# Optimization experiments

Measured on AMD Instinct MI355X. Metric: run time of the kernel, lower is better.

## Reference

```python
import jax, jax.numpy as jnp
import numpy as np

B, S, D_IN, D_OUT, N, R = 8, 4096, 1280, 1280, 4, 16


def setup_inputs() -> dict:
    key = jax.random.key(0)
    ks = jax.random.split(key, 7)
    x = jax.random.normal(ks[0], (B, S, D_IN), dtype=jnp.float32)
    W = jax.random.normal(ks[1], (D_OUT, D_IN), dtype=jnp.float32) * 0.02
    bias = jax.random.normal(ks[2], (D_OUT,), dtype=jnp.float32) * 0.02
    A = jax.random.normal(ks[3], (N, R, D_IN), dtype=jnp.float32) * 0.02
    Bw = jax.random.normal(ks[4], (N, D_OUT, R), dtype=jnp.float32) * 0.02
    scalings = jax.random.uniform(ks[5], (N,), dtype=jnp.float32)
    masks = jax.random.uniform(ks[6], (N, S), dtype=jnp.float32)
    # normalize masks to sum ~1 per position, per docstring
    masks = masks / jnp.sum(masks, axis=0, keepdims=True)
    return {"x": x, "W": W, "bias": bias, "A": A, "Bw": Bw,
            "scalings": scalings, "masks": masks}


def reference(x, W, bias, A, Bw, scalings, masks):
    # base linear: y = x @ W^T + b
    base = jnp.einsum('bsd,od->bso', x, W) + bias
    # batched LoRA branches: h = x @ A_i^T  (b,s,n,r)
    h = jnp.einsum('bsd,nrd->bsnr', x, A)
    # lora_out_i = h @ B_i^T  (b,s,n,o)
    lora = jnp.einsum('bsnr,nor->bsno', h, Bw)
    # weighted sum over subjects: scaling_i * mask_i(pos)
    lora_sum = jnp.einsum('bsno,n,ns->bso', lora, scalings, masks)
    return base + lora_sum
```

## Files before the change

kernel.cpp:

```cpp
#include <hip/hip_runtime.h>
#include <hip/hip_bf16.h>
#include <stdint.h>

#define S_LEN   4096
#define DIN     1280
#define DOUT    1280
#define N_LORA  4
#define R_LORA  16
#define M_TOT   32768
#define KC      (DIN + N_LORA*R_LORA)
#define NR      64

typedef __attribute__((ext_vector_type(4))) float floatx4;
typedef __attribute__((ext_vector_type(8))) short shortx8;

typedef union { uint4 u; shortx8 s; } punx8;

static __device__ __forceinline__ unsigned short bf16_rne(float f) {
    union { float f; unsigned u; } v; v.f = f;
    unsigned u = v.u;
    u += 0x7fffu + ((u >> 16) & 1u);
    return (unsigned short)(u >> 16);
}

static __device__ __forceinline__ void async16(const unsigned short* g, unsigned short* l) {
    __builtin_amdgcn_global_load_lds(
        (const __attribute__((address_space(1))) unsigned int*)g,
        (__attribute__((address_space(3))) unsigned int*)l, 16, 0, 0);
}

static __device__ __forceinline__ uint4 cvt8(const float* src) {
    const float4* p = (const float4*)src;
    float4 a = p[0], b = p[1];
    uint4 o;
    o.x = (unsigned)bf16_rne(a.x) | ((unsigned)bf16_rne(a.y) << 16);
    o.y = (unsigned)bf16_rne(a.z) | ((unsigned)bf16_rne(a.w) << 16);
    o.z = (unsigned)bf16_rne(b.x) | ((unsigned)bf16_rne(b.y) << 16);
    o.w = (unsigned)bf16_rne(b.z) | ((unsigned)bf16_rne(b.w) << 16);
    return o;
}

#define VMCNT(n) asm volatile("s_waitcnt vmcnt(" #n ")" ::: "memory")
#define LGKM0    do { asm volatile("s_waitcnt lgkmcnt(0)" ::: "memory"); \
                      __builtin_amdgcn_sched_barrier(0); } while (0)
static __device__ __forceinline__ void barx() {
    asm volatile("" ::: "memory");
    __builtin_amdgcn_s_barrier();
    asm volatile("" ::: "memory");
}

__global__ __launch_bounds__(256) void k_build_wcat(const float* __restrict__ W,
                                                    const float* __restrict__ Bw,
                                                    unsigned short* __restrict__ Wcat) {
    int i = blockIdx.x * 256 + threadIdx.x;
    int e = i * 8;
    int o = e / KC;
    int c = e - o * KC;
    const float* src;
    if (c < DIN) {
        src = W + o * DIN + c;
    } else {
        int j = c - DIN;
        int n = j >> 4, r = j & 15;
        src = Bw + (n * DOUT + o) * R_LORA + r;
    }
    *(uint4*)(Wcat + o * KC + c) = cvt8(src);
}

__global__ __launch_bounds__(256) void k_convert_abp(const float* __restrict__ A,
                                                     unsigned short* __restrict__ Abp) {
    int step = blockIdx.x;
    int t = threadIdx.x;
    int ct = t >> 6, lane = t & 63;
    int mi = lane & 15, kq = lane >> 4;
    const float* src = A + (ct * 16 + mi) * DIN + step * 32 + kq * 8;
    *(uint4*)(Abp + ((size_t)(step * 4 + ct) * 64 + lane) * 8) = cvt8(src);
}

__global__ __launch_bounds__(1024) void k_lora_g(const float* __restrict__ x,
                                                 const unsigned short* __restrict__ Abp,
                                                 const float* __restrict__ scalings,
                                                 const float* __restrict__ masks,
                                                 unsigned short* __restrict__ g,
                                                 unsigned short* __restrict__ xb) {
    __shared__ float hs[4][64][64];
    int tid = threadIdx.x;
    int wave = tid >> 6, lane = tid & 63;
    int kg = wave >> 2, wv = wave & 3;
    int mi = lane & 15, kq = lane >> 4;
    int m0 = blockIdx.x * 64;

    const float* xrow = x + (size_t)(m0 + wv * 16 + mi) * DIN;
    unsigned short* xbrow = xb + (size_t)(m0 + wv * 16 + mi) * DIN;

    floatx4 acc[4] = {};
    for (int s = 0; s < 10; ++s) {
        int step = kg * 10 + s;
        int k = step * 32 + kq * 8;
        punx8 xp; xp.u = cvt8(xrow + k);
        *(uint4*)(xbrow + k) = xp.u;
        shortx8 xf = xp.s;
#pragma unroll
        for (int ct = 0; ct < 4; ++ct) {
            shortx8 bfr = *(const shortx8*)(Abp + ((size_t)(step * 4 + ct) * 64 + lane) * 8);
            acc[ct] = __builtin_amdgcn_mfma_f32_16x16x32_bf16(xf, bfr, acc[ct], 0, 0, 0);
        }
    }
#pragma unroll
    for (int ct = 0; ct < 4; ++ct)
#pragma unroll
        for (int reg = 0; reg < 4; ++reg)
            hs[kg][wv * 16 + kq * 4 + reg][ct * 16 + mi] = acc[ct][reg];
    __syncthreads();

    int r = tid >> 4;
    int c0 = (tid & 15) * 4;
    float4 s0 = *(const float4*)&hs[0][r][c0];
    float4 s1 = *(const float4*)&hs[1][r][c0];
    float4 s2 = *(const float4*)&hs[2][r][c0];
    float4 s3 = *(const float4*)&hs[3][r][c0];
    int n = c0 >> 4;
    int m = m0 + r;
    float wgt = scalings[n] * masks[n * S_LEN + (m & (S_LEN - 1))];
    float v0 = (s0.x + s1.x + s2.x + s3.x) * wgt;
    float v1 = (s0.y + s1.y + s2.y + s3.y) * wgt;
    float v2 = (s0.z + s1.z + s2.z + s3.z) * wgt;
    float v3 = (s0.w + s1.w + s2.w + s3.w) * wgt;
    uint2 packed;
    packed.x = (unsigned)bf16_rne(v0) | ((unsigned)bf16_rne(v1) << 16);
    packed.y = (unsigned)bf16_rne(v2) | ((unsigned)bf16_rne(v3) << 16);
    *(uint2*)(g + (size_t)m * NR + c0) = packed;
}

__global__ __launch_bounds__(512, 2) void k_main_gemm(const unsigned short* __restrict__ xb,
                                                      const unsigned short* __restrict__ g,
                                                      const unsigned short* __restrict__ Wcat,
                                                      const float* __restrict__ bias,
                                                      float* __restrict__ out) {
    __shared__ alignas(16) unsigned short As[2][256 * 64];
    __shared__ alignas(16) unsigned short Bs[2][256 * 64];

    const int tid = threadIdx.x;
    const int wave = tid >> 6, lane = tid & 63;
    const int wm = wave >> 2, wn = wave & 3;
    const int mi = lane & 15, kq = lane >> 4;

    int bx = blockIdx.x;
    int xcd = bx & 7, slot = bx >> 3;
    int srb = slot / 5;
    const int m0 = (xcd * 16 + srb) * 256;
    const int n0 = (slot - srb * 5) * 256;

    const int tr = tid >> 3;
    const int ts = (tid & 7) ^ (tr & 7);

    const unsigned short* pA = xb   + (size_t)(m0 + tr) * DIN + ts * 8;
    const unsigned short* pG = g    + (size_t)(m0 + tr) * NR  + ts * 8;
    const unsigned short* pB = Wcat + (size_t)(n0 + tr) * KC  + ts * 8;

    const int swz  = mi & 7;
    const int loK0 = mi * 128 + (((0) + kq) ^ swz) * 16;
    const int loK1 = mi * 128 + (((4) + kq) ^ swz) * 16;
    const int rbA  = (wm * 128) * 128;
    const int rbB  = (wn * 64) * 128;

    floatx4 acc[8][4] = {};
    shortx8 aR[2][8];
    shortx8 b[2][4];

    auto stA = [&](int t, int h) {
        unsigned short* d = &As[t & 1][(h * 128) * 64 + tid * 8];
        if (t < 20) {
            const unsigned short* s = pA + (size_t)(h * 128) * DIN + t * 64;
            async16(s, d);
            async16(s + (size_t)64 * DIN, d + 64 * 64);
        } else {
            const unsigned short* s = pG + (size_t)(h * 128) * NR;
            async16(s, d);
            async16(s + (size_t)64 * NR, d + 64 * 64);
        }
    };
    auto stB = [&](int t, int h) {
        const unsigned short* s = pB + (size_t)(h * 128) * KC + t * 64;
        unsigned short* d = &Bs[t & 1][(h * 128) * 64 + tid * 8];
        async16(s, d);
        async16(s + (size_t)64 * KC, d + 64 * 64);
    };

#define READ_A(bufb, mh)  _Pragma("unroll") \
    for (int fm = 0; fm < 4; ++fm) { \
        const char* p = (const char*)As[bufb] + rbA + ((mh) * 64 + fm * 16) * 128; \
        aR[(mh)][fm * 2 + 0] = *(const shortx8*)(p + loK0); \
        aR[(mh)][fm * 2 + 1] = *(const shortx8*)(p + loK1); \
    }
#define READ_B(bufb, nh)  _Pragma("unroll") \
    for (int fn = 0; fn < 2; ++fn) { \
        const char* p = (const char*)Bs[bufb] + rbB + ((nh) * 32 + fn * 16) * 128; \
        b[nh][fn * 2 + 0] = *(const shortx8*)(p + loK0); \
        b[nh][fn * 2 + 1] = *(const shortx8*)(p + loK1); \
    }
#define MFMA16(mh, nh)  do { __builtin_amdgcn_s_setprio(1); \
    _Pragma("unroll") \
    for (int fm = 0; fm < 4; ++fm) \
        _Pragma("unroll") \
        for (int fn = 0; fn < 2; ++fn) { \
            acc[(mh)*4+fm][(nh)*2+fn] = __builtin_amdgcn_mfma_f32_16x16x32_bf16( \
                aR[(mh)][fm*2+0], b[nh][fn*2+0], acc[(mh)*4+fm][(nh)*2+fn], 0, 0, 0); \
            acc[(mh)*4+fm][(nh)*2+fn] = __builtin_amdgcn_mfma_f32_16x16x32_bf16( \
                aR[(mh)][fm*2+1], b[nh][fn*2+1], acc[(mh)*4+fm][(nh)*2+fn], 0, 0, 0); \
        } \
    __builtin_amdgcn_s_setprio(0); } while (0)

    stA(0, 0); stA(0, 1); stB(0, 0); stB(0, 1);
    stB(1, 0); stB(1, 1); stA(1, 0);
    VMCNT(6);
    barx();
    READ_A(0, 0); READ_B(0, 0);

    for (int it = 0; it < 10; ++it) {
        const int T1 = 2 * it + 1, N0 = 2 * it + 2, N1 = 2 * it + 3;
        const bool lastI = (it == 9);

        barx();
        stA(T1, 1);
        LGKM0;
        READ_B(0, 1);
        MFMA16(0, 0);
        barx();
        LGKM0;
        READ_A(0, 1);
        MFMA16(0, 1);
        barx();
        stB(N0, 0);
        LGKM0;
        MFMA16(1, 0);
        VMCNT(2);
        barx();
        stB(N0, 1); stA(N0, 0);
        LGKM0;
        READ_A(1, 0); READ_B(1, 0);
        MFMA16(1, 1);
        barx();
        stA(N0, 1);
        LGKM0;
        READ_B(1, 1);
        MFMA16(0, 0);
        barx();
        LGKM0;
        READ_A(1, 1);
        MFMA16(0, 1);
        barx();
        if (!lastI) stB(N1, 0);
        LGKM0;
        MFMA16(1, 0);
        if (lastI) { VMCNT(0); } else { VMCNT(2); }
        barx();
        if (!lastI) { stB(N1, 1); stA(N1, 0); }
        LGKM0;
        READ_A(0, 0); READ_B(0, 0);
        MFMA16(1, 1);
    }

    LGKM0;
    READ_B(0, 1);
    MFMA16(0, 0);
    LGKM0;
    READ_A(0, 1);
    MFMA16(0, 1);
    LGKM0;
    MFMA16(1, 0);
    MFMA16(1, 1);

    float bv[4];
#pragma unroll
    for (int nf = 0; nf < 4; ++nf)
        bv[nf] = bias[n0 + wn * 64 + (nf >> 1) * 32 + (nf & 1) * 16 + mi];
#pragma unroll
    for (int mf = 0; mf < 8; ++mf) {
        const int row = m0 + wm * 128 + (mf >> 2) * 64 + (mf & 3) * 16 + kq * 4;
#pragma unroll
        for (int nf = 0; nf < 4; ++nf) {
            const int col = n0 + wn * 64 + (nf >> 1) * 32 + (nf & 1) * 16 + mi;
            float* op = out + (size_t)row * DOUT + col;
#pragma unroll
            for (int reg = 0; reg < 4; ++reg)
                op[(size_t)reg * DOUT] = acc[mf][nf][reg] + bv[nf];
        }
    }
#undef READ_A
#undef READ_B
#undef MFMA16
}

extern "C" void kernel_launch(void* const* d_in, const int* in_sizes, int n_in,
                              void* d_out, int out_size, void* d_ws, size_t ws_size,
                              hipStream_t stream) {
    const float* x     = (const float*)d_in[0];
    const float* W     = (const float*)d_in[1];
    const float* bias  = (const float*)d_in[2];
    const float* A     = (const float*)d_in[3];
    const float* Bw    = (const float*)d_in[4];
    const float* scal  = (const float*)d_in[5];
    const float* masks = (const float*)d_in[6];
    float* out = (float*)d_out;

    unsigned short* xb   = (unsigned short*)d_ws;
    unsigned short* g    = xb + (size_t)M_TOT * DIN;
    unsigned short* Wcat = g + (size_t)M_TOT * NR;
    unsigned short* Abp  = Wcat + (size_t)DOUT * KC;

    k_build_wcat<<<(DOUT * KC) / (8 * 256), 256, 0, stream>>>(W, Bw, Wcat);
    k_convert_abp<<<DIN / 32, 256, 0, stream>>>(A, Abp);
    k_lora_g<<<M_TOT / 64, 1024, 0, stream>>>(x, Abp, scal, masks, g, xb);
    k_main_gemm<<<(M_TOT / 256) * (DOUT / 256), 512, 0, stream>>>(xb, g, Wcat, bias, out);
}
```

Baseline: 455.2 us.

## Restructure GEMM main loop into barrier-separated read/MFMA phases with single A fragment

Rewrites the software-pipelined main loop of the fused base+LoRA GEMM. Each LDS read group and each MFMA group now sits in its own barrier-delimited phase, so waves alternate between memory and compute. The explicit lgkmcnt waits and sched barriers are removed, and the A register buffer shrinks from two halves to one to save VGPRs. This adds many more workgroup barriers per iteration and leaves LDS-read waits to the compiler. It also drops the overlap where one half's fragment was loaded while the previous MFMAs ran, and changes the vmcnt thresholds.

```diff
diff --git a/kernel.cpp b/kernel.cpp
--- a/kernel.cpp
+++ b/kernel.cpp
@@ -41,8 +41,6 @@
 }
 
 #define VMCNT(n) asm volatile("s_waitcnt vmcnt(" #n ")" ::: "memory")
-#define LGKM0    do { asm volatile("s_waitcnt lgkmcnt(0)" ::: "memory"); \
-                      __builtin_amdgcn_sched_barrier(0); } while (0)
 static __device__ __forceinline__ void barx() {
     asm volatile("" ::: "memory");
     __builtin_amdgcn_s_barrier();
@@ -165,7 +163,7 @@
     const int rbB  = (wn * 64) * 128;
 
     floatx4 acc[8][4] = {};
-    shortx8 aR[2][8];
+    shortx8 a[8];
     shortx8 b[2][4];
 
     auto stA = [&](int t, int h) {
@@ -190,8 +188,8 @@
 #define READ_A(bufb, mh)  _Pragma("unroll") \
     for (int fm = 0; fm < 4; ++fm) { \
         const char* p = (const char*)As[bufb] + rbA + ((mh) * 64 + fm * 16) * 128; \
-        aR[(mh)][fm * 2 + 0] = *(const shortx8*)(p + loK0); \
-        aR[(mh)][fm * 2 + 1] = *(const shortx8*)(p + loK1); \
+        a[fm * 2 + 0] = *(const shortx8*)(p + loK0); \
+        a[fm * 2 + 1] = *(const shortx8*)(p + loK1); \
     }
 #define READ_B(bufb, nh)  _Pragma("unroll") \
     for (int fn = 0; fn < 2; ++fn) { \
@@ -205,9 +203,9 @@
         _Pragma("unroll") \
         for (int fn = 0; fn < 2; ++fn) { \
             acc[(mh)*4+fm][(nh)*2+fn] = __builtin_amdgcn_mfma_f32_16x16x32_bf16( \
-                aR[(mh)][fm*2+0], b[nh][fn*2+0], acc[(mh)*4+fm][(nh)*2+fn], 0, 0, 0); \
+                a[fm*2+0], b[nh][fn*2+0], acc[(mh)*4+fm][(nh)*2+fn], 0, 0, 0); \
             acc[(mh)*4+fm][(nh)*2+fn] = __builtin_amdgcn_mfma_f32_16x16x32_bf16( \
-                aR[(mh)][fm*2+1], b[nh][fn*2+1], acc[(mh)*4+fm][(nh)*2+fn], 0, 0, 0); \
+                a[fm*2+1], b[nh][fn*2+1], acc[(mh)*4+fm][(nh)*2+fn], 0, 0, 0); \
         } \
     __builtin_amdgcn_s_setprio(0); } while (0)
 
@@ -215,59 +213,56 @@
     stB(1, 0); stB(1, 1); stA(1, 0);
     VMCNT(6);
     barx();
-    READ_A(0, 0); READ_B(0, 0);
 
     for (int it = 0; it < 10; ++it) {
         const int T1 = 2 * it + 1, N0 = 2 * it + 2, N1 = 2 * it + 3;
         const bool lastI = (it == 9);
 
-        barx();
+        READ_A(0, 0); READ_B(0, 0);
         stA(T1, 1);
-        LGKM0;
+        barx();
+        MFMA16(0, 0);
+        barx();
         READ_B(0, 1);
+        barx();
+        MFMA16(0, 1);
+        barx();
+        READ_A(0, 1);
+        stB(N0, 0);
+        barx();
+        MFMA16(1, 0);
+        barx();
+        stB(N0, 1); stA(N0, 0);
+        barx();
+        MFMA16(1, 1);
+        VMCNT(6);
+        barx();
+        READ_A(1, 0); READ_B(1, 0);
+        stA(N0, 1);
+        barx();
         MFMA16(0, 0);
         barx();
-        LGKM0;
-        READ_A(0, 1);
+        READ_B(1, 1);
+        barx();
         MFMA16(0, 1);
         barx();
-        stB(N0, 0);
-        LGKM0;
+        READ_A(1, 1);
+        if (!lastI) stB(N1, 0);
+        barx();
         MFMA16(1, 0);
-        VMCNT(2);
-        barx();
-        stB(N0, 1); stA(N0, 0);
-        LGKM0;
-        READ_A(1, 0); READ_B(1, 0);
+        barx();
+        if (!lastI) { stB(N1, 1); stA(N1, 0); }
+        barx();
         MFMA16(1, 1);
-        barx();
-        stA(N0, 1);
-        LGKM0;
-        READ_B(1, 1);
-        MFMA16(0, 0);
-        barx();
-        LGKM0;
-        READ_A(1, 1);
-        MFMA16(0, 1);
-        barx();
-        if (!lastI) stB(N1, 0);
-        LGKM0;
-        MFMA16(1, 0);
-        if (lastI) { VMCNT(0); } else { VMCNT(2); }
-        barx();
-        if (!lastI) { stB(N1, 1); stA(N1, 0); }
-        LGKM0;
-        READ_A(0, 0); READ_B(0, 0);
-        MFMA16(1, 1);
-    }
-
-    LGKM0;
+        if (lastI) { VMCNT(0); } else { VMCNT(6); }
+        barx();
+    }
+
+    READ_A(0, 0); READ_B(0, 0);
+    MFMA16(0, 0);
     READ_B(0, 1);
-    MFMA16(0, 0);
-    LGKM0;
+    MFMA16(0, 1);
     READ_A(0, 1);
-    MFMA16(0, 1);
-    LGKM0;
     MFMA16(1, 0);
     MFMA16(1, 1);
 
```

After: 449.0 us. No clear change (-1.3%).

## Replace hand-interleaved eight-phase pipeline with simple double-buffered K loop

Applied to the files above, without the earlier changes.

Removes the hand-scheduled eight-phase main loop, its explicit lgkmcnt waits and sched barriers. In their place is a plain double-buffered loop that issues all async loads for the next K tile, reads the current tile's fragments, runs the MFMAs, then waits on vmcnt(0) and one barrier per tile. This cuts barrier count and code complexity and lets the compiler schedule LDS reads. In exchange it loses the fine-grained overlap and prefetch depth of the older schedule, and it fully drains global loads every iteration.

```diff
diff --git a/kernel.cpp b/kernel.cpp
--- a/kernel.cpp
+++ b/kernel.cpp
@@ -41,8 +41,6 @@
 }
 
 #define VMCNT(n) asm volatile("s_waitcnt vmcnt(" #n ")" ::: "memory")
-#define LGKM0    do { asm volatile("s_waitcnt lgkmcnt(0)" ::: "memory"); \
-                      __builtin_amdgcn_sched_barrier(0); } while (0)
 static __device__ __forceinline__ void barx() {
     asm volatile("" ::: "memory");
     __builtin_amdgcn_s_barrier();
@@ -199,7 +197,7 @@
         b[nh][fn * 2 + 0] = *(const shortx8*)(p + loK0); \
         b[nh][fn * 2 + 1] = *(const shortx8*)(p + loK1); \
     }
-#define MFMA16(mh, nh)  do { __builtin_amdgcn_s_setprio(1); \
+#define MFMA16(mh, nh)  do { \
     _Pragma("unroll") \
     for (int fm = 0; fm < 4; ++fm) \
         _Pragma("unroll") \
@@ -209,67 +207,33 @@
             acc[(mh)*4+fm][(nh)*2+fn] = __builtin_amdgcn_mfma_f32_16x16x32_bf16( \
                 aR[(mh)][fm*2+1], b[nh][fn*2+1], acc[(mh)*4+fm][(nh)*2+fn], 0, 0, 0); \
         } \
-    __builtin_amdgcn_s_setprio(0); } while (0)
+    } while (0)
 
     stA(0, 0); stA(0, 1); stB(0, 0); stB(0, 1);
-    stB(1, 0); stB(1, 1); stA(1, 0);
-    VMCNT(6);
+    VMCNT(0);
     barx();
-    READ_A(0, 0); READ_B(0, 0);
-
-    for (int it = 0; it < 10; ++it) {
-        const int T1 = 2 * it + 1, N0 = 2 * it + 2, N1 = 2 * it + 3;
-        const bool lastI = (it == 9);
-
+
+    for (int t = 0; t < 21; ++t) {
+        const int cur = t & 1;
+        if (t < 20) {
+            stA(t + 1, 0); stA(t + 1, 1);
+            stB(t + 1, 0); stB(t + 1, 1);
+        }
+        READ_A(cur, 0);
+        READ_B(cur, 0);
+        READ_B(cur, 1);
+        __builtin_amdgcn_s_setprio(1);
+        MFMA16(0, 0);
+        MFMA16(0, 1);
+        __builtin_amdgcn_s_setprio(0);
+        READ_A(cur, 1);
+        __builtin_amdgcn_s_setprio(1);
+        MFMA16(1, 0);
+        MFMA16(1, 1);
+        __builtin_amdgcn_s_setprio(0);
+        VMCNT(0);
         barx();
-        stA(T1, 1);
-        LGKM0;
-        READ_B(0, 1);
-        MFMA16(0, 0);
-        barx();
-        LGKM0;
-        READ_A(0, 1);
-        MFMA16(0, 1);
-        barx();
-        stB(N0, 0);
-        LGKM0;
-        MFMA16(1, 0);
-        VMCNT(2);
-        barx();
-        stB(N0, 1); stA(N0, 0);
-        LGKM0;
-        READ_A(1, 0); READ_B(1, 0);
-        MFMA16(1, 1);
-        barx();
-        stA(N0, 1);
-        LGKM0;
-        READ_B(1, 1);
-        MFMA16(0, 0);
-        barx();
-        LGKM0;
-        READ_A(1, 1);
-        MFMA16(0, 1);
-        barx();
-        if (!lastI) stB(N1, 0);
-        LGKM0;
-        MFMA16(1, 0);
-        if (lastI) { VMCNT(0); } else { VMCNT(2); }
-        barx();
-        if (!lastI) { stB(N1, 1); stA(N1, 0); }
-        LGKM0;
-        READ_A(0, 0); READ_B(0, 0);
-        MFMA16(1, 1);
-    }
-
-    LGKM0;
-    READ_B(0, 1);
-    MFMA16(0, 0);
-    LGKM0;
-    READ_A(0, 1);
-    MFMA16(0, 1);
-    LGKM0;
-    MFMA16(1, 0);
-    MFMA16(1, 1);
+    }
 
     float bv[4];
 #pragma unroll
```

Result: slower. 475.7 us (+4.5%).
